# Optimization experiments

Hardware: AMD Instinct MI355X
Metric: run time of the kernel (lower is better)

## Reference

```python
import jax, jax.numpy as jnp
import numpy as np

SCALING_FACTOR = 1.8
K = 10
ALPHA = 0.15
EPS = 1e-12


def setup_inputs() -> dict:
    key = jax.random.key(0)
    k1, k2, k3, k4 = jax.random.split(key, 4)
    N, E, IN, OUT = 100000, 3200000, 512, 256
    x = jax.random.normal(k1, (N, IN), dtype=jnp.float32)
    edge_index = jax.random.randint(k2, (2, E), 0, N, dtype=jnp.int64)
    W1 = jax.random.normal(k3, (OUT, IN), dtype=jnp.float32) * (1.0 / np.sqrt(IN))
    b1 = jax.random.normal(k4, (OUT,), dtype=jnp.float32) * 0.01
    return {"x": x, "edge_index": edge_index, "W1": W1, "b1": b1}


def _gcn_norm(edge_index, num_nodes):
    # add self-loops (PyG gcn_norm default), symmetric D^-1/2 (A+I) D^-1/2
    loops = jnp.arange(num_nodes, dtype=edge_index.dtype)
    src = jnp.concatenate([edge_index[0], loops])
    dst = jnp.concatenate([edge_index[1], loops])
    deg = jax.ops.segment_sum(jnp.ones_like(dst, dtype=jnp.float32), dst,
                              num_segments=num_nodes)
    dinv = jnp.where(deg > 0, jax.lax.rsqrt(deg), 0.0)
    norm = dinv[src] * dinv[dst]  # [E+N]
    return src, dst, norm


def reference(x, edge_index, W1, b1):
    N = x.shape[0]
    # linear1
    h = jnp.einsum('ni,oi->no', x, W1) + b1  # [N, OUT]
    # F.normalize(p=2, dim=1) * scaling_factor
    nrm = jnp.sqrt(jnp.sum(h * h, axis=1, keepdims=True))
    h = h / jnp.maximum(nrm, EPS) * SCALING_FACTOR
    # APPNP K=10, alpha=0.15
    src, dst, norm = _gcn_norm(edge_index, N)
    h0 = h

    def step(z, _):
        msg = z[src] * norm[:, None]                       # gather + scale
        agg = jax.ops.segment_sum(msg, dst, num_segments=N)  # scatter-add
        z = (1.0 - ALPHA) * agg + ALPHA * h0
        return z, None

    z, _ = jax.lax.scan(step, h, None, length=K)
    return z
```

## Files before the change

kernel.cpp:

```cpp
#include <hip/hip_runtime.h>
#include <hip/hip_fp16.h>


#define ALPHA 0.15f
#define BETA 0.85f
#define SCALE 1.8f

typedef _Float16 f16x8 __attribute__((ext_vector_type(8)));
typedef float f32x4 __attribute__((ext_vector_type(4)));

__global__ void convert_w(const float* __restrict__ W1, _Float16* __restrict__ Wh) {
    int i = blockIdx.x * blockDim.x + threadIdx.x;
    if (i < 256 * 512) Wh[i] = (_Float16)W1[i];
}

__global__ __launch_bounds__(256) void gemm_f16(
    const float* __restrict__ A, const _Float16* __restrict__ Wh,
    const float* __restrict__ bias, float* __restrict__ C, int M) {
    __shared__ _Float16 As[64][72];
    const int tid  = threadIdx.x;
    const int wv   = tid >> 6;
    const int lane = tid & 63;
    const int lc   = lane & 15;
    const int lr   = lane >> 4;
    const int m0   = blockIdx.x * 64;
    const int n0w  = wv * 64;

    f32x4 acc[4][4];
#pragma unroll
    for (int i = 0; i < 4; i++)
#pragma unroll
        for (int j = 0; j < 4; j++) {
            acc[i][j][0] = 0.f; acc[i][j][1] = 0.f;
            acc[i][j][2] = 0.f; acc[i][j][3] = 0.f;
        }

    const int srow = tid >> 2;
    const int sseg = tid & 3;
    const bool inb = (m0 + srow) < M;

    for (int k0 = 0; k0 < 512; k0 += 64) {
        float4 av0, av1, av2, av3;
        if (inb) {
            const float4* ap = (const float4*)(A + (size_t)(m0 + srow) * 512 + k0 + sseg * 16);
            av0 = ap[0]; av1 = ap[1]; av2 = ap[2]; av3 = ap[3];
        } else {
            av0 = av1 = av2 = av3 = make_float4(0.f, 0.f, 0.f, 0.f);
        }
        if (k0) __syncthreads();
        f16x8 p0, p1;
        p0[0] = (_Float16)av0.x; p0[1] = (_Float16)av0.y;
        p0[2] = (_Float16)av0.z; p0[3] = (_Float16)av0.w;
        p0[4] = (_Float16)av1.x; p0[5] = (_Float16)av1.y;
        p0[6] = (_Float16)av1.z; p0[7] = (_Float16)av1.w;
        p1[0] = (_Float16)av2.x; p1[1] = (_Float16)av2.y;
        p1[2] = (_Float16)av2.z; p1[3] = (_Float16)av2.w;
        p1[4] = (_Float16)av3.x; p1[5] = (_Float16)av3.y;
        p1[6] = (_Float16)av3.z; p1[7] = (_Float16)av3.w;
        _Float16* wp = &As[srow][sseg * 16];
        *(f16x8*)wp = p0;
        *(f16x8*)(wp + 8) = p1;
        __syncthreads();

        f16x8 bf[2][4];
#pragma unroll
        for (int s = 0; s < 2; ++s)
#pragma unroll
            for (int nt = 0; nt < 4; ++nt)
                bf[s][nt] = *(const f16x8*)(Wh + (size_t)(n0w + nt * 16 + lc) * 512
                                            + k0 + s * 32 + lr * 8);

#pragma unroll
        for (int s = 0; s < 2; ++s) {
            f16x8 af[4];
#pragma unroll
            for (int mt = 0; mt < 4; ++mt)
                af[mt] = *(const f16x8*)&As[mt * 16 + lc][s * 32 + lr * 8];
#pragma unroll
            for (int mt = 0; mt < 4; ++mt)
#pragma unroll
                for (int nt = 0; nt < 4; ++nt)
                    acc[mt][nt] = __builtin_amdgcn_mfma_f32_16x16x32_f16(
                        af[mt], bf[s][nt], acc[mt][nt], 0, 0, 0);
        }
    }

    float bv[4];
#pragma unroll
    for (int nt = 0; nt < 4; ++nt) bv[nt] = bias[n0w + nt * 16 + lc];
#pragma unroll
    for (int mt = 0; mt < 4; ++mt)
#pragma unroll
        for (int r = 0; r < 4; ++r) {
            int m = m0 + mt * 16 + lr * 4 + r;
            if (m < M) {
                float* cp = C + (size_t)m * 256 + n0w + lc;
#pragma unroll
                for (int nt = 0; nt < 4; ++nt)
                    cp[nt * 16] = acc[mt][nt][r] + bv[nt];
            }
        }
}

__global__ __launch_bounds__(256) void normalize_kernel(
    const float* __restrict__ h, const float* __restrict__ dinv,
    __half* __restrict__ h16, __half* __restrict__ y0, int N) {
    int n = blockIdx.x;
    if (n >= N) return;
    int t = threadIdx.x;
    float v = h[(size_t)n * 256 + t];
    float ss = v * v;
#pragma unroll
    for (int off = 32; off > 0; off >>= 1) ss += __shfl_down(ss, off, 64);
    __shared__ float wsum[4];
    int w = t >> 6, lane = t & 63;
    if (lane == 0) wsum[w] = ss;
    __syncthreads();
    float tot = wsum[0] + wsum[1] + wsum[2] + wsum[3];
    float nrm = sqrtf(tot);
    float s = SCALE / fmaxf(nrm, 1e-12f);
    float hv = v * s;
    h16[(size_t)n * 256 + t] = __float2half(hv);
    y0[(size_t)n * 256 + t] = __float2half(hv * dinv[n]);
}

__global__ void init_counts(int* __restrict__ counts, int N) {
    int i = blockIdx.x * blockDim.x + threadIdx.x;
    if (i < N) counts[i] = 1;
}

__global__ void count_kernel(const int* __restrict__ dst, int* __restrict__ counts, int E) {
    int i = blockIdx.x * blockDim.x + threadIdx.x;
    if (i < E) atomicAdd(&counts[dst[i]], 1);
}

__global__ void dinv_kernel(const int* __restrict__ counts, float* __restrict__ dinv, int N) {
    int i = blockIdx.x * blockDim.x + threadIdx.x;
    if (i < N) dinv[i] = rsqrtf((float)counts[i]);
}

__global__ __launch_bounds__(256) void scan_phase1(
    const int* __restrict__ counts, int* __restrict__ offsets,
    int* __restrict__ blocksums, int N) {
    __shared__ int sdata[256];
    int b = blockIdx.x;
    int base = b * 1024;
    int t = threadIdx.x;
    int v[4];
    int idx0 = base + t * 4;
    int sum = 0;
#pragma unroll
    for (int j = 0; j < 4; j++) {
        int i = idx0 + j;
        v[j] = (i < N) ? counts[i] : 0;
        sum += v[j];
    }
    sdata[t] = sum;
    __syncthreads();
    for (int off = 1; off < 256; off <<= 1) {
        int x = (t >= off) ? sdata[t - off] : 0;
        __syncthreads();
        sdata[t] += x;
        __syncthreads();
    }
    int incl = sdata[t];
    int excl = incl - sum;
    if (t == 255) blocksums[b] = incl;
    int run = excl;
#pragma unroll
    for (int j = 0; j < 4; j++) {
        int i = idx0 + j;
        if (i < N) offsets[i] = run;
        run += v[j];
    }
}

__global__ __launch_bounds__(128) void scan_phase2(int* __restrict__ blocksums, int nb) {
    __shared__ int s[128];
    int t = threadIdx.x;
    int v = (t < nb) ? blocksums[t] : 0;
    s[t] = v;
    __syncthreads();
    for (int off = 1; off < 128; off <<= 1) {
        int x = (t >= off) ? s[t - off] : 0;
        __syncthreads();
        s[t] += x;
        __syncthreads();
    }
    if (t < nb) blocksums[t] = s[t] - v;
}

__global__ void scan_phase3(int* __restrict__ offsets, const int* __restrict__ blocksums,
                            int* __restrict__ cursor, int N, int total) {
    int i = blockIdx.x * blockDim.x + threadIdx.x;
    if (i < N) {
        int o = offsets[i] + blocksums[i >> 10];
        offsets[i] = o;
        cursor[i] = o;
    }
    if (i == N) offsets[N] = total;
}

__global__ void fill_kernel(const int* __restrict__ src, const int* __restrict__ dst,
                            int* __restrict__ cursor, int* __restrict__ col, int E, int N) {
    int i = blockIdx.x * blockDim.x + threadIdx.x;
    int tot = E + N;
    if (i >= tot) return;
    int s, d;
    if (i < E) { s = src[i]; d = dst[i]; }
    else       { s = d = i - E; }
    int p = atomicAdd(&cursor[d], 1);
    col[p] = s;
}

__device__ __forceinline__ void acc_half4(float4& a, float2 r) {
    union { float2 f; __half2 h[2]; } u;
    u.f = r;
    float2 lo = __half22float2(u.h[0]);
    float2 hi = __half22float2(u.h[1]);
    a.x += lo.x; a.y += lo.y; a.z += hi.x; a.w += hi.y;
}

template <bool FINAL>
__global__ __launch_bounds__(256) void spmm_kernel(
    const __half* __restrict__ yin, const __half* __restrict__ h16,
    const int* __restrict__ offs, const int* __restrict__ col,
    const float* __restrict__ dinv, void* __restrict__ outp, int N) {
    int gw = blockIdx.x * 4 + (threadIdx.x >> 6);
    if (gw >= N) return;
    int lane = threadIdx.x & 63;
    int beg = offs[gw], end = offs[gw + 1];

    float4 a0 = make_float4(0.f, 0.f, 0.f, 0.f);
    float4 a1 = make_float4(0.f, 0.f, 0.f, 0.f);
    float4 a2 = make_float4(0.f, 0.f, 0.f, 0.f);
    float4 a3 = make_float4(0.f, 0.f, 0.f, 0.f);

    int e = beg;
    for (; e + 3 < end; e += 4) {
        int s0 = __builtin_nontemporal_load(col + e);
        int s1 = __builtin_nontemporal_load(col + e + 1);
        int s2 = __builtin_nontemporal_load(col + e + 2);
        int s3 = __builtin_nontemporal_load(col + e + 3);
        float2 r0 = ((const float2*)(yin + (size_t)s0 * 256))[lane];
        float2 r1 = ((const float2*)(yin + (size_t)s1 * 256))[lane];
        float2 r2 = ((const float2*)(yin + (size_t)s2 * 256))[lane];
        float2 r3 = ((const float2*)(yin + (size_t)s3 * 256))[lane];
        acc_half4(a0, r0); acc_half4(a1, r1); acc_half4(a2, r2); acc_half4(a3, r3);
    }
    for (; e < end; ++e) {
        int s0 = __builtin_nontemporal_load(col + e);
        float2 r0 = ((const float2*)(yin + (size_t)s0 * 256))[lane];
        acc_half4(a0, r0);
    }

    float dg = dinv[gw];
    float wd = BETA * dg;

    const float* hp = (const float*)(h16 + (size_t)gw * 256) + lane * 2;
    float hx = __builtin_nontemporal_load(hp);
    float hy = __builtin_nontemporal_load(hp + 1);
    float4 hh;
    {
        union { float f; __half2 h; } ux, uy;
        ux.f = hx; uy.f = hy;
        float2 lo = __half22float2(ux.h);
        float2 hi = __half22float2(uy.h);
        hh.x = lo.x; hh.y = lo.y; hh.z = hi.x; hh.w = hi.y;
    }

    float4 o;
    o.x = wd * (a0.x + a1.x + a2.x + a3.x) + ALPHA * hh.x;
    o.y = wd * (a0.y + a1.y + a2.y + a3.y) + ALPHA * hh.y;
    o.z = wd * (a0.z + a1.z + a2.z + a3.z) + ALPHA * hh.z;
    o.w = wd * (a0.w + a1.w + a2.w + a3.w) + ALPHA * hh.w;

    if (FINAL) {
        float* op = (float*)outp + (size_t)gw * 256 + lane * 4;
        __builtin_nontemporal_store(o.x, op);
        __builtin_nontemporal_store(o.y, op + 1);
        __builtin_nontemporal_store(o.z, op + 2);
        __builtin_nontemporal_store(o.w, op + 3);
    } else {
        __half2 p0 = __floats2half2_rn(o.x * dg, o.y * dg);
        __half2 p1 = __floats2half2_rn(o.z * dg, o.w * dg);
        union { float f; __half2 h; } u0, u1;
        u0.h = p0; u1.h = p1;
        float* op = (float*)((__half*)outp + (size_t)gw * 256) + lane * 2;
        __builtin_nontemporal_store(u0.f, op);
        __builtin_nontemporal_store(u1.f, op + 1);
    }
}

extern "C" void kernel_launch(void* const* d_in, const int* in_sizes, int n_in,
                              void* d_out, int out_size, void* d_ws, size_t ws_size,
                              hipStream_t stream) {
    const float* x  = (const float*)d_in[0];
    const int* ei   = (const int*)d_in[1];
    const float* W1 = (const float*)d_in[2];
    const float* b1 = (const float*)d_in[3];
    float* out = (float*)d_out;

    const int N = in_sizes[0] / 512;
    const int E = in_sizes[1] / 2;
    const int* src = ei;
    const int* dst = ei + E;
    const int NNZ = E + N;

    char* w = (char*)d_ws;
    float* h0 = (float*)w;      w += (size_t)N * 256 * 4;
    __half* h16 = (__half*)w;   w += (size_t)N * 256 * 2;
    __half* y0 = (__half*)w;    w += (size_t)N * 256 * 2;
    __half* yB = (__half*)w;    w += (size_t)N * 256 * 2;
    _Float16* Wh = (_Float16*)w; w += (size_t)256 * 512 * 2;
    float* dinv = (float*)w;    w += (size_t)N * 4;
    int* counts = (int*)w;      w += (size_t)N * 4;
    int* offsets = (int*)w;     w += (size_t)(N + 64) * 4;
    int* blocksums = (int*)w;   w += 128 * 4;
    int* col = (int*)w;         w += (size_t)NNZ * 4;
    __half* yA = (__half*)h0;

    init_counts<<<(N + 255) / 256, 256, 0, stream>>>(counts, N);
    count_kernel<<<(E + 255) / 256, 256, 0, stream>>>(dst, counts, E);
    dinv_kernel<<<(N + 255) / 256, 256, 0, stream>>>(counts, dinv, N);
    convert_w<<<(256 * 512 + 255) / 256, 256, 0, stream>>>(W1, Wh);
    gemm_f16<<<(N + 63) / 64, 256, 0, stream>>>(x, Wh, b1, h0, N);
    normalize_kernel<<<N, 256, 0, stream>>>(h0, dinv, h16, y0, N);
    int nb = (N + 1023) / 1024;
    scan_phase1<<<nb, 256, 0, stream>>>(counts, offsets, blocksums, N);
    scan_phase2<<<1, 128, 0, stream>>>(blocksums, nb);
    scan_phase3<<<(N + 256) / 256, 256, 0, stream>>>(offsets, blocksums, counts, N, NNZ);
    fill_kernel<<<(NNZ + 255) / 256, 256, 0, stream>>>(src, dst, counts, col, E, N);
    int nblk = (N + 3) / 4;
    const __half* cur = y0;
    for (int it = 0; it < 9; ++it) {
        __half* nxt = (it & 1) ? yB : yA;
        spmm_kernel<false><<<nblk, 256, 0, stream>>>(cur, h16, offsets, col, dinv,
                                                     (void*)nxt, N);
        cur = nxt;
    }
    spmm_kernel<true><<<nblk, 256, 0, stream>>>(cur, h16, offsets, col, dinv,
                                                (void*)out, N);
}
```

Before: 3.209 ms.

## Partition count and fill atomics by destination range per XCD

Replaces the per-edge count and CSR fill kernels with 512-block versions. Each block reads a chunk of edges but only applies atomics to destinations in one eighth of the node range, selected by blockIdx mod 8. The aim is for blocks on the same XCD to touch the same disjoint slice of counters, keeping atomics local to one L2 and avoiding cross-die coherence traffic. In exchange every edge is read eight times, and self-loop insertion moves into the chunk-0 blocks.

```diff
diff --git a/kernel.cpp b/kernel.cpp
--- a/kernel.cpp
+++ b/kernel.cpp
@@ -129,9 +129,30 @@
     if (i < N) counts[i] = 1;
 }
 
-__global__ void count_kernel(const int* __restrict__ dst, int* __restrict__ counts, int E) {
-    int i = blockIdx.x * blockDim.x + threadIdx.x;
-    if (i < E) atomicAdd(&counts[dst[i]], 1);
+__global__ __launch_bounds__(256) void count_xcd(
+    const int* __restrict__ dst, int* __restrict__ counts, int E, int N) {
+    const int b = blockIdx.x, x = b & 7, c = b >> 3;
+    const int NC = gridDim.x >> 3;
+    const int lo = (int)(((long long)x * N) >> 3);
+    const int hi = (int)(((long long)(x + 1) * N) >> 3);
+    const int csz = (((E + NC - 1) / NC) + 3) & ~3;
+    const int e0 = c * csz;
+    const int e1 = min(e0 + csz, E);
+    const int rem = (e1 > e0) ? (e1 - e0) : 0;
+    const int t = threadIdx.x;
+    const int nvec = ((E & 3) == 0) ? (rem >> 2) : 0;
+    for (int i = t; i < nvec; i += 256) {
+        const int e = e0 + (i << 2);
+        int4 d4 = *(const int4*)(dst + e);
+        if (d4.x >= lo && d4.x < hi) atomicAdd(&counts[d4.x], 1);
+        if (d4.y >= lo && d4.y < hi) atomicAdd(&counts[d4.y], 1);
+        if (d4.z >= lo && d4.z < hi) atomicAdd(&counts[d4.z], 1);
+        if (d4.w >= lo && d4.w < hi) atomicAdd(&counts[d4.w], 1);
+    }
+    for (int e = e0 + (nvec << 2) + t; e < e1; e += 256) {
+        int d = dst[e];
+        if (d >= lo && d < hi) atomicAdd(&counts[d], 1);
+    }
 }
 
 __global__ void dinv_kernel(const int* __restrict__ counts, float* __restrict__ dinv, int N) {
@@ -201,16 +222,37 @@
     if (i == N) offsets[N] = total;
 }
 
-__global__ void fill_kernel(const int* __restrict__ src, const int* __restrict__ dst,
-                            int* __restrict__ cursor, int* __restrict__ col, int E, int N) {
-    int i = blockIdx.x * blockDim.x + threadIdx.x;
-    int tot = E + N;
-    if (i >= tot) return;
-    int s, d;
-    if (i < E) { s = src[i]; d = dst[i]; }
-    else       { s = d = i - E; }
-    int p = atomicAdd(&cursor[d], 1);
-    col[p] = s;
+__global__ __launch_bounds__(256) void fill_xcd(
+    const int* __restrict__ src, const int* __restrict__ dst,
+    int* __restrict__ cursor, int* __restrict__ col, int E, int N) {
+    const int b = blockIdx.x, x = b & 7, c = b >> 3;
+    const int NC = gridDim.x >> 3;
+    const int lo = (int)(((long long)x * N) >> 3);
+    const int hi = (int)(((long long)(x + 1) * N) >> 3);
+    const int csz = (((E + NC - 1) / NC) + 3) & ~3;
+    const int e0 = c * csz;
+    const int e1 = min(e0 + csz, E);
+    const int rem = (e1 > e0) ? (e1 - e0) : 0;
+    const int t = threadIdx.x;
+    const int nvec = ((E & 3) == 0) ? (rem >> 2) : 0;
+    for (int i = t; i < nvec; i += 256) {
+        const int e = e0 + (i << 2);
+        int4 d4 = *(const int4*)(dst + e);
+        if (d4.x >= lo && d4.x < hi) { int p = atomicAdd(&cursor[d4.x], 1); col[p] = src[e]; }
+        if (d4.y >= lo && d4.y < hi) { int p = atomicAdd(&cursor[d4.y], 1); col[p] = src[e + 1]; }
+        if (d4.z >= lo && d4.z < hi) { int p = atomicAdd(&cursor[d4.z], 1); col[p] = src[e + 2]; }
+        if (d4.w >= lo && d4.w < hi) { int p = atomicAdd(&cursor[d4.w], 1); col[p] = src[e + 3]; }
+    }
+    for (int e = e0 + (nvec << 2) + t; e < e1; e += 256) {
+        int d = dst[e];
+        if (d >= lo && d < hi) { int p = atomicAdd(&cursor[d], 1); col[p] = src[e]; }
+    }
+    if (c == 0) {
+        for (int n = lo + t; n < hi; n += 256) {
+            int p = atomicAdd(&cursor[n], 1);
+            col[p] = n;
+        }
+    }
 }
 
 __device__ __forceinline__ void acc_half4(float4& a, float2 r) {
@@ -321,7 +363,7 @@
     __half* yA = (__half*)h0;
 
     init_counts<<<(N + 255) / 256, 256, 0, stream>>>(counts, N);
-    count_kernel<<<(E + 255) / 256, 256, 0, stream>>>(dst, counts, E);
+    count_xcd<<<512, 256, 0, stream>>>(dst, counts, E, N);
     dinv_kernel<<<(N + 255) / 256, 256, 0, stream>>>(counts, dinv, N);
     convert_w<<<(256 * 512 + 255) / 256, 256, 0, stream>>>(W1, Wh);
     gemm_f16<<<(N + 63) / 64, 256, 0, stream>>>(x, Wh, b1, h0, N);
@@ -330,7 +372,7 @@
     scan_phase1<<<nb, 256, 0, stream>>>(counts, offsets, blocksums, N);
     scan_phase2<<<1, 128, 0, stream>>>(blocksums, nb);
     scan_phase3<<<(N + 256) / 256, 256, 0, stream>>>(offsets, blocksums, counts, N, NNZ);
-    fill_kernel<<<(NNZ + 255) / 256, 256, 0, stream>>>(src, dst, counts, col, E, N);
+    fill_xcd<<<512, 256, 0, stream>>>(src, dst, counts, col, E, N);
     int nblk = (N + 3) / 4;
     const __half* cur = y0;
     for (int it = 0; it < 9; ++it) {
```

Measured after the change: 3.165 ms. Within noise of the previous version (-1.4%).
